# Performance work log

Measured on AMD Instinct MI355X. Metric: run time of the kernel, lower is better.

## Reference

```python
import jax, jax.numpy as jnp
import numpy as np

D_MODEL = 512
D_INNER = 1024   # expand * d_model
NH = 16          # heads (headdim 64)
HD = 64
NS = 16          # d_state
HID = 1024       # ff hidden = expand * d_model


def _ln(x, w, b, eps=1e-5):
    m = x.mean(-1, keepdims=True)
    v = ((x - m) ** 2).mean(-1, keepdims=True)
    return (x - m) * jax.lax.rsqrt(v + eps) * w + b


def _rms(x, w, eps=1e-5):
    return x * jax.lax.rsqrt((x * x).mean(-1, keepdims=True) + eps) * w


def _tree_scan(dt, xh, Bv, Cv, pidx, A):
    # dt:[B,T,W,H] xh:[B,T,W,H,P] Bv,Cv:[B,T,W,N] pidx:[B,T,W] A:[H]
    B_, T, W, H = dt.shape
    P = xh.shape[-1]
    N = Bv.shape[-1]
    h0 = jnp.zeros((B_, W, H, P, N), dt.dtype)
    xs = (jnp.moveaxis(dt, 1, 0), jnp.moveaxis(xh, 1, 0),
          jnp.moveaxis(Bv, 1, 0), jnp.moveaxis(Cv, 1, 0),
          jnp.moveaxis(pidx, 1, 0))

    def step(h, inp):
        dt_t, xh_t, b_t, c_t, p_t = inp
        # gather parent state from previous level along the width axis
        hp = jnp.take_along_axis(h, p_t[:, :, None, None, None], axis=1)  # [B,W,H,P,N]
        dA = jnp.exp(dt_t * A)                                            # [B,W,H]
        h_new = dA[..., None, None] * hp \
              + dt_t[..., None, None] * xh_t[..., None] * b_t[:, :, None, None, :]
        y_t = jnp.einsum('bwhpn,bwn->bwhp', h_new, c_t)
        return h_new, y_t

    _, ys = jax.lax.scan(step, h0, xs)
    return jnp.moveaxis(ys, 0, 1)  # [B,T,W,H,P]


def setup_inputs() -> dict:
    key = jax.random.key(0)
    ks = jax.random.split(key, 12)
    B, T, W = 8, 64, 16
    d_in_proj = 2 * D_INNER + 2 * NS + NH  # z | x | B | C | dt
    inp = {
        'x': jax.random.normal(ks[0], (B, T, W, D_MODEL), jnp.float32),
        'parent_pos': jax.random.randint(ks[1], (B, T, W), 0, W, dtype=jnp.int32),
        'ln1_w': jnp.ones((D_MODEL,), jnp.float32),
        'ln1_b': jnp.zeros((D_MODEL,), jnp.float32),
        'in_w': jax.random.normal(ks[2], (D_MODEL, d_in_proj), jnp.float32) * 0.02,
        'in_b': jnp.zeros((d_in_proj,), jnp.float32),
        'A_log': jnp.log(jax.random.uniform(ks[3], (NH,), jnp.float32, 1.0, 16.0)),
        'dt_bias': jnp.full((NH,), -4.0, jnp.float32),
        'Dp': jnp.ones((NH,), jnp.float32),
        'norm_w': jnp.ones((D_INNER,), jnp.float32),
        'out_w': jax.random.normal(ks[4], (D_INNER, D_MODEL), jnp.float32) * 0.02,
        'out_b': jnp.zeros((D_MODEL,), jnp.float32),
        'ln2_w': jnp.ones((D_MODEL,), jnp.float32),
        'ln2_b': jnp.zeros((D_MODEL,), jnp.float32),
        'ff1_w': jax.random.normal(ks[5], (D_MODEL, 2 * HID), jnp.float32) * 0.02,
        'ff1_b': jnp.zeros((2 * HID,), jnp.float32),
        'ff2_w': jax.random.normal(ks[6], (HID, D_MODEL), jnp.float32) * 0.02,
        'ff2_b': jnp.zeros((D_MODEL,), jnp.float32),
    }
    return inp


def reference(x, parent_pos, ln1_w, ln1_b, in_w, in_b, A_log, dt_bias, Dp,
              norm_w, out_w, out_b, ln2_w, ln2_b, ff1_w, ff1_b, ff2_w, ff2_b):
    # norm1 + TreeMamba2 + residual
    xn = _ln(x, ln1_w, ln1_b)
    proj = xn @ in_w + in_b
    z, xp, Bv, Cv, dtr = jnp.split(
        proj, [D_INNER, 2 * D_INNER, 2 * D_INNER + NS, 2 * D_INNER + 2 * NS], axis=-1)
    dt = jax.nn.softplus(dtr + dt_bias)            # [B,T,W,NH]
    A = -jnp.exp(A_log)                            # [NH]
    xh = xp.reshape(*xp.shape[:-1], NH, HD)        # [B,T,W,NH,HD]
    y = _tree_scan(dt, xh, Bv, Cv, parent_pos, A)  # [B,T,W,NH,HD]
    y = y + Dp[..., None] * xh                     # skip connection D*x
    y = y.reshape(*y.shape[:-2], D_INNER)
    y = _rms(y * jax.nn.silu(z), norm_w)           # gated RMSNorm
    y = y @ out_w + out_b
    x = y + x
    # norm2 + gated FF + residual
    yn = _ln(x, ln2_w, ln2_b)
    f = yn @ ff1_w + ff1_b
    f1, g = jnp.split(f, 2, axis=-1)
    f = (f1 * jax.nn.silu(g)) @ ff2_w + ff2_b
    return x + f
```

## Files before the change

### kernel.cpp

```cpp
#include <hip/hip_runtime.h>
#include <hip/hip_bf16.h>
#include <cmath>

#define D_MODEL 512
#define D_INNER 1024
#define NHEAD 16
#define HDIM 64
#define NSTATE 16
#define NB 8
#define NT 64
#define NW 16
#define MROWS 8192
#define PROJ_LD 2176
#define NPROJ 2096

typedef __attribute__((ext_vector_type(8))) short short8;
typedef __attribute__((ext_vector_type(4))) float f32x4;
typedef __hip_bfloat16 bf16;
typedef unsigned int u32;

__device__ __forceinline__ u32 fbits(float f) { return __float_as_uint(f); }
__device__ __forceinline__ float ubits(u32 u) { return __uint_as_float(u); }
__device__ __forceinline__ u32 pack_bf(float a, float b) {
  return (fbits(b) & 0xffff0000u) | (fbits(a) >> 16);
}

__device__ __forceinline__ float block_sum(float v, float* sbuf) {
#pragma unroll
  for (int o = 32; o > 0; o >>= 1) v += __shfl_down(v, o, 64);
  int lane = threadIdx.x & 63, wid = threadIdx.x >> 6;
  if (lane == 0) sbuf[wid] = v;
  __syncthreads();
  if (threadIdx.x == 0) {
    float t = 0.f;
    for (int i = 0; i < 4; i++) t += sbuf[i];
    sbuf[0] = t;
  }
  __syncthreads();
  return sbuf[0];
}

__global__ __launch_bounds__(256) void ln512_bf16_kernel(
    const float* __restrict__ x, const float* __restrict__ w,
    const float* __restrict__ b, bf16* __restrict__ out) {
  __shared__ float s1[8], s2[8];
  int row = blockIdx.x;
  const float* xr = x + (size_t)row * D_MODEL;
  bf16* outr = out + (size_t)row * D_MODEL;
  int c0 = threadIdx.x, c1 = threadIdx.x + 256;
  float v0 = xr[c0], v1 = xr[c1];
  float s  = block_sum(v0 + v1, s1);
  float ss = block_sum(v0 * v0 + v1 * v1, s2);
  float mean = s * (1.f / 512.f);
  float var  = ss * (1.f / 512.f) - mean * mean;
  float inv  = rsqrtf(var + 1e-5f);
  outr[c0] = __float2bfloat16((v0 - mean) * inv * w[c0] + b[c0]);
  outr[c1] = __float2bfloat16((v1 - mean) * inv * w[c1] + b[c1]);
}

__global__ __launch_bounds__(256) void wconv_t_kernel(
    const float* __restrict__ w, bf16* __restrict__ wt,
    int K, int N, int Npad) {
  __shared__ float tile[32][33];
  int n0 = blockIdx.x * 32, k0 = blockIdx.y * 32;
  int tx = threadIdx.x & 31, ty = threadIdx.x >> 5;
#pragma unroll
  for (int i = 0; i < 4; i++) {
    int k = k0 + ty + i * 8, n = n0 + tx;
    tile[ty + i * 8][tx] = (k < K && n < N) ? w[(size_t)k * N + n] : 0.f;
  }
  __syncthreads();
#pragma unroll
  for (int i = 0; i < 4; i++) {
    int n = n0 + ty + i * 8, k = k0 + tx;
    if (n < Npad && k < K) wt[(size_t)n * K + k] = __float2bfloat16(tile[tx][ty + i * 8]);
  }
}

template<int BM, int BN, int WN, int MR, int NR>
__global__ __launch_bounds__(256) void mfma_gemm_kernel(
    const bf16* __restrict__ A, const bf16* __restrict__ Bt,
    const float* __restrict__ bias, int nbias,
    const float* __restrict__ resid,
    float* __restrict__ C, int ldc, int K) {
  constexpr int ROWS = BM + BN;
  constexpr int ISS  = ROWS / 64;
  __shared__ __align__(16) bf16 sAB[2][ROWS][32];

  int wid = threadIdx.x >> 6, lane = threadIdx.x & 63;
  int row0 = blockIdx.y * BM, col0 = blockIdx.x * BN;
  int wr = (wid / WN) * (MR * 16);
  int wc = (wid % WN) * (NR * 16);
  int lr = lane >> 2;
  int lc = (lane & 3) * 8;

  f32x4 acc[MR][NR];
#pragma unroll
  for (int m = 0; m < MR; m++)
#pragma unroll
    for (int n = 0; n < NR; n++) acc[m][n] = (f32x4){0.f, 0.f, 0.f, 0.f};

  auto stage = [&](int buf, int k0) {
#pragma unroll
    for (int i = 0; i < ISS; i++) {
      int rb = (wid * ISS + i) * 16;
      int r = rb + lr;
      const bf16* src = (r < BM)
          ? A  + (size_t)(row0 + r) * K + k0 + lc
          : Bt + (size_t)(col0 + (r - BM)) * K + k0 + lc;
      __builtin_amdgcn_global_load_lds(
          (const __attribute__((address_space(1))) void*)src,
          (__attribute__((address_space(3))) void*)&sAB[buf][rb][0], 16, 0, 0);
    }
  };

  stage(0, 0);
  asm volatile("s_waitcnt vmcnt(0)" ::: "memory");
  __syncthreads();

  int cur = 0;
  for (int k0 = 0; k0 < K; k0 += 32, cur ^= 1) {
    if (k0 + 32 < K) stage(cur ^ 1, k0 + 32);
    short8 a[MR], b[NR];
    int kk = (lane >> 4) * 8;
#pragma unroll
    for (int m = 0; m < MR; m++)
      a[m] = *(const short8*)&sAB[cur][wr + m * 16 + (lane & 15)][kk];
#pragma unroll
    for (int n = 0; n < NR; n++)
      b[n] = *(const short8*)&sAB[cur][BM + wc + n * 16 + (lane & 15)][kk];
#pragma unroll
    for (int m = 0; m < MR; m++)
#pragma unroll
      for (int n = 0; n < NR; n++)
        acc[m][n] = __builtin_amdgcn_mfma_f32_16x16x32_bf16(a[m], b[n], acc[m][n], 0, 0, 0);
    asm volatile("s_waitcnt vmcnt(0)" ::: "memory");
    __syncthreads();
  }

  int crow = row0 + wr + (lane >> 4) * 4;
  int ccol = col0 + wc + (lane & 15);
#pragma unroll
  for (int m = 0; m < MR; m++) {
#pragma unroll
    for (int n = 0; n < NR; n++) {
      int colg = ccol + n * 16;
      float bv = bias ? ((colg < nbias) ? bias[colg] : 0.f) : 0.f;
#pragma unroll
      for (int j = 0; j < 4; j++) {
        int rowg = crow + m * 16 + j;
        float v = acc[m][n][j] + bv;
        if (resid) v += resid[(size_t)rowg * ldc + colg];
        C[(size_t)rowg * ldc + colg] = v;
      }
    }
  }
}

__global__ __launch_bounds__(256) void inproj_gemm_kernel(
    const bf16* __restrict__ A, const bf16* __restrict__ Bt,
    const float* __restrict__ bias,
    bf16* __restrict__ Cb, float* __restrict__ aux, int K) {
  constexpr int BM = 128, ROWS = 256, ISS = 4;
  __shared__ __align__(16) bf16 sAB[2][ROWS][32];

  int wid = threadIdx.x >> 6, lane = threadIdx.x & 63;
  int row0 = blockIdx.y * BM, col0 = blockIdx.x * 128;
  int wr = (wid >> 1) * 64;
  int wc = (wid & 1) * 64;
  int lr = lane >> 2;
  int lc = (lane & 3) * 8;

  f32x4 acc[4][4];
#pragma unroll
  for (int m = 0; m < 4; m++)
#pragma unroll
    for (int n = 0; n < 4; n++) acc[m][n] = (f32x4){0.f, 0.f, 0.f, 0.f};

  auto stage = [&](int buf, int k0) {
#pragma unroll
    for (int i = 0; i < ISS; i++) {
      int rb = (wid * ISS + i) * 16;
      int r = rb + lr;
      const bf16* src = (r < BM)
          ? A  + (size_t)(row0 + r) * K + k0 + lc
          : Bt + (size_t)(col0 + (r - BM)) * K + k0 + lc;
      __builtin_amdgcn_global_load_lds(
          (const __attribute__((address_space(1))) void*)src,
          (__attribute__((address_space(3))) void*)&sAB[buf][rb][0], 16, 0, 0);
    }
  };

  stage(0, 0);
  asm volatile("s_waitcnt vmcnt(0)" ::: "memory");
  __syncthreads();

  int cur = 0;
  for (int k0 = 0; k0 < K; k0 += 32, cur ^= 1) {
    if (k0 + 32 < K) stage(cur ^ 1, k0 + 32);
    short8 a[4], b[4];
    int kk = (lane >> 4) * 8;
#pragma unroll
    for (int m = 0; m < 4; m++)
      a[m] = *(const short8*)&sAB[cur][wr + m * 16 + (lane & 15)][kk];
#pragma unroll
    for (int n = 0; n < 4; n++)
      b[n] = *(const short8*)&sAB[cur][BM + wc + n * 16 + (lane & 15)][kk];
#pragma unroll
    for (int m = 0; m < 4; m++)
#pragma unroll
      for (int n = 0; n < 4; n++)
        acc[m][n] = __builtin_amdgcn_mfma_f32_16x16x32_bf16(a[m], b[n], acc[m][n], 0, 0, 0);
    asm volatile("s_waitcnt vmcnt(0)" ::: "memory");
    __syncthreads();
  }

  int crow = row0 + wr + (lane >> 4) * 4;
  int ccol = col0 + wc + (lane & 15);
#pragma unroll
  for (int m = 0; m < 4; m++) {
#pragma unroll
    for (int n = 0; n < 4; n++) {
      int colg = ccol + n * 16;
      float bv = (colg < NPROJ) ? bias[colg] : 0.f;
#pragma unroll
      for (int j = 0; j < 4; j++) {
        int rowg = crow + m * 16 + j;
        float v = acc[m][n][j] + bv;
        Cb[(size_t)rowg * PROJ_LD + colg] = __float2bfloat16(v);
        if (colg >= 2048 && colg < 2112)
          aux[(size_t)rowg * 64 + (colg - 2048)] = v;
      }
    }
  }
}

__global__ __launch_bounds__(256) void ff1_fused_kernel(
    const bf16* __restrict__ A, const bf16* __restrict__ Bt,
    const float* __restrict__ bias, bf16* __restrict__ out, int K) {
  constexpr int BM = 128, ROWS = 384, ISS = 6;
  __shared__ __align__(16) bf16 sAB[2][ROWS][32];

  int wid = threadIdx.x >> 6, lane = threadIdx.x & 63;
  int row0 = blockIdx.y * BM, col0 = blockIdx.x * 128;
  int wr = (wid >> 1) * 64;
  int wc = (wid & 1) * 64;
  int lr = lane >> 2;
  int lc = (lane & 3) * 8;

  f32x4 acc1[4][4], acc2[4][4];
#pragma unroll
  for (int m = 0; m < 4; m++)
#pragma unroll
    for (int n = 0; n < 4; n++) {
      acc1[m][n] = (f32x4){0.f, 0.f, 0.f, 0.f};
      acc2[m][n] = (f32x4){0.f, 0.f, 0.f, 0.f};
    }

  auto stage = [&](int buf, int k0) {
#pragma unroll
    for (int i = 0; i < ISS; i++) {
      int rb = (wid * ISS + i) * 16;
      int r = rb + lr;
      const bf16* src;
      if (r < BM)       src = A  + (size_t)(row0 + r) * K + k0 + lc;
      else if (r < 256) src = Bt + (size_t)(col0 + (r - 128)) * K + k0 + lc;
      else              src = Bt + (size_t)(1024 + col0 + (r - 256)) * K + k0 + lc;
      __builtin_amdgcn_global_load_lds(
          (const __attribute__((address_space(1))) void*)src,
          (__attribute__((address_space(3))) void*)&sAB[buf][rb][0], 16, 0, 0);
    }
  };

  stage(0, 0);
  asm volatile("s_waitcnt vmcnt(0)" ::: "memory");
  __syncthreads();

  int cur = 0;
  for (int k0 = 0; k0 < K; k0 += 32, cur ^= 1) {
    if (k0 + 32 < K) stage(cur ^ 1, k0 + 32);
    short8 a[4], b1[4], b2[4];
    int kk = (lane >> 4) * 8;
#pragma unroll
    for (int m = 0; m < 4; m++)
      a[m] = *(const short8*)&sAB[cur][wr + m * 16 + (lane & 15)][kk];
#pragma unroll
    for (int n = 0; n < 4; n++) {
      b1[n] = *(const short8*)&sAB[cur][128 + wc + n * 16 + (lane & 15)][kk];
      b2[n] = *(const short8*)&sAB[cur][256 + wc + n * 16 + (lane & 15)][kk];
    }
#pragma unroll
    for (int m = 0; m < 4; m++)
#pragma unroll
      for (int n = 0; n < 4; n++) {
        acc1[m][n] = __builtin_amdgcn_mfma_f32_16x16x32_bf16(a[m], b1[n], acc1[m][n], 0, 0, 0);
        acc2[m][n] = __builtin_amdgcn_mfma_f32_16x16x32_bf16(a[m], b2[n], acc2[m][n], 0, 0, 0);
      }
    asm volatile("s_waitcnt vmcnt(0)" ::: "memory");
    __syncthreads();
  }

  int crow = row0 + wr + (lane >> 4) * 4;
  int ccol = col0 + wc + (lane & 15);
#pragma unroll
  for (int m = 0; m < 4; m++) {
#pragma unroll
    for (int n = 0; n < 4; n++) {
      int colg = ccol + n * 16;
      float bv1 = bias[colg];
      float bv2 = bias[1024 + colg];
#pragma unroll
      for (int j = 0; j < 4; j++) {
        int rowg = crow + m * 16 + j;
        float f1 = acc1[m][n][j] + bv1;
        float g  = acc2[m][n][j] + bv2;
        float sg = g / (1.f + expf(-g));
        out[(size_t)rowg * 1024 + colg] = __float2bfloat16(f1 * sg);
      }
    }
  }
}

__global__ __launch_bounds__(256) void tree_scan_kernel(
    const bf16* __restrict__ xb, const float* __restrict__ aux,
    const int* __restrict__ parent,
    const float* __restrict__ A_log, const float* __restrict__ dt_bias,
    const float* __restrict__ Dp, bf16* __restrict__ y) {
  const int tid = threadIdx.x;
  const int ps = blockIdx.x & 3;
  const int h  = (blockIdx.x >> 2) & 15;
  const int b  = blockIdx.x >> 6;
  const int wid = tid >> 6;
  const int lane = tid & 63;
  const int w = lane >> 2;
  const int q = lane & 3;
  const int pl = wid * 4 + q;

  __shared__ __align__(16) u32   BCs[8][16][20];
  __shared__ __align__(16) float dAs[16][8];
  __shared__ __align__(16) float dtss[16][8];
  __shared__ __align__(16) int   pars[16][8];

  const float Ah  = -expf(A_log[h]);
  const float dtb = dt_bias[h];
  const float Dh  = Dp[h];
  const int xcol = 1024 + (h << 6) + (ps << 4) + pl;
  const int ycol = (h << 6) + (ps << 4) + pl;

  float hst[16];
#pragma unroll
  for (int n = 0; n < 16; n++) hst[n] = 0.f;

  const int sp_t = (tid >> 1) >> 4, sp_w = (tid >> 1) & 15, sp_h = tid & 1;

  for (int c = 0; c < 8; c++) {
    const int t0 = c * 8;
    __syncthreads();
    float xv[8];
#pragma unroll
    for (int tt = 0; tt < 8; tt++) {
      size_t row = ((size_t)(b * NT + t0 + tt)) * NW + w;
      xv[tt] = __bfloat162float(xb[row * PROJ_LD + xcol]);
    }
    if (tid < 128) {
      int t = tid >> 4, wv = tid & 15;
      size_t row = ((size_t)(b * NT + t0 + t)) * NW + wv;
      float dtr = aux[row * 64 + 32 + h] + dtb;
      float dtv = (dtr > 20.f) ? dtr : log1pf(expf(dtr));
      dtss[wv][t] = dtv;
      dAs[wv][t]  = expf(dtv * Ah);
      pars[wv][t] = parent[row];
    }
    {
      size_t row = ((size_t)(b * NT + t0 + sp_t)) * NW + sp_w;
      const float* src = aux + row * 64 + sp_h * 16;
      float4 v0 = *(const float4*)&src[0];
      float4 v1 = *(const float4*)&src[4];
      float4 v2 = *(const float4*)&src[8];
      float4 v3 = *(const float4*)&src[12];
      uint4 p0 = {pack_bf(v0.x, v0.y), pack_bf(v0.z, v0.w),
                  pack_bf(v1.x, v1.y), pack_bf(v1.z, v1.w)};
      uint4 p1 = {pack_bf(v2.x, v2.y), pack_bf(v2.z, v2.w),
                  pack_bf(v3.x, v3.y), pack_bf(v3.z, v3.w)};
      *(uint4*)&BCs[sp_t][sp_w][sp_h * 8]     = p0;
      *(uint4*)&BCs[sp_t][sp_w][sp_h * 8 + 4] = p1;
    }
    __syncthreads();
    float dAr[8], dtr8[8];
    int parr[8];
    *(float4*)&dAr[0]  = *(const float4*)&dAs[w][0];
    *(float4*)&dAr[4]  = *(const float4*)&dAs[w][4];
    *(float4*)&dtr8[0] = *(const float4*)&dtss[w][0];
    *(float4*)&dtr8[4] = *(const float4*)&dtss[w][4];
    *(int4*)&parr[0]   = *(const int4*)&pars[w][0];
    *(int4*)&parr[4]   = *(const int4*)&pars[w][4];

#pragma unroll
    for (int tt = 0; tt < 8; tt++) {
      float dA  = dAr[tt];
      float dtx = dtr8[tt] * xv[tt];
      int   par = parr[tt];
      int gidx = (((par << 2) | q) << 2);
      u32 pk[8];
#pragma unroll
      for (int i = 0; i < 8; i++)
        pk[i] = (u32)__builtin_amdgcn_ds_bpermute(
            gidx, (int)pack_bf(hst[2 * i], hst[2 * i + 1]));
      uint4 bA = *(const uint4*)&BCs[tt][w][0];
      uint4 bB = *(const uint4*)&BCs[tt][w][4];
      uint4 cA = *(const uint4*)&BCs[tt][w][8];
      uint4 cB = *(const uint4*)&BCs[tt][w][12];
      const u32* bw = (const u32*)&bA;
      u32 bwv[8] = {bA.x, bA.y, bA.z, bA.w, bB.x, bB.y, bB.z, bB.w};
      u32 cwv[8] = {cA.x, cA.y, cA.z, cA.w, cB.x, cB.y, cB.z, cB.w};
      (void)bw;
      float yv = 0.f;
#pragma unroll
      for (int i = 0; i < 8; i++) {
        u32 g = pk[i], bu = bwv[i], cu = cwv[i];
        float hp0 = ubits(g << 16),  hp1 = ubits(g & 0xffff0000u);
        float bl  = ubits(bu << 16), bh  = ubits(bu & 0xffff0000u);
        float cl  = ubits(cu << 16), ch  = ubits(cu & 0xffff0000u);
        float h0 = fmaf(dA, hp0, dtx * bl);
        float h1 = fmaf(dA, hp1, dtx * bh);
        hst[2 * i] = h0;
        hst[2 * i + 1] = h1;
        yv = fmaf(h0, cl, fmaf(h1, ch, yv));
      }
      size_t row = ((size_t)(b * NT + t0 + tt)) * NW + w;
      y[row * D_INNER + ycol] = __float2bfloat16(fmaf(Dh, xv[tt], yv));
    }
  }
}

__global__ __launch_bounds__(256) void gate_rms_kernel(
    const bf16* __restrict__ yin, const bf16* __restrict__ projb,
    const float* __restrict__ norm_w, bf16* __restrict__ out) {
  __shared__ float sbuf[8];
  int row = blockIdx.x;
  const bf16* yr = yin + (size_t)row * D_INNER;
  const bf16* zr = projb + (size_t)row * PROJ_LD;
  int c = threadIdx.x * 4;
  bf16 y4[4], z4[4];
  *(uint2*)y4 = *(const uint2*)&yr[c];
  *(uint2*)z4 = *(const uint2*)&zr[c];
  float gv[4];
  float ss = 0.f;
#pragma unroll
  for (int j = 0; j < 4; j++) {
    float z = __bfloat162float(z4[j]);
    float t = __bfloat162float(y4[j]) * (z / (1.f + expf(-z)));
    gv[j] = t;
    ss += t * t;
  }
  ss = block_sum(ss, sbuf);
  float scale = rsqrtf(ss * (1.f / 1024.f) + 1e-5f);
  bf16 o4[4];
#pragma unroll
  for (int j = 0; j < 4; j++) o4[j] = __float2bfloat16(gv[j] * scale * norm_w[c + j]);
  *(uint2*)&out[(size_t)row * D_INNER + c] = *(uint2*)o4;
}

extern "C" void kernel_launch(void* const* d_in, const int* in_sizes, int n_in,
                              void* d_out, int out_size, void* d_ws, size_t ws_size,
                              hipStream_t stream) {
  const float* x       = (const float*)d_in[0];
  const int*   parent  = (const int*)d_in[1];
  const float* ln1_w   = (const float*)d_in[2];
  const float* ln1_b   = (const float*)d_in[3];
  const float* in_w    = (const float*)d_in[4];
  const float* in_b    = (const float*)d_in[5];
  const float* A_log   = (const float*)d_in[6];
  const float* dt_bias = (const float*)d_in[7];
  const float* Dp      = (const float*)d_in[8];
  const float* norm_w  = (const float*)d_in[9];
  const float* out_w   = (const float*)d_in[10];
  const float* out_b   = (const float*)d_in[11];
  const float* ln2_w   = (const float*)d_in[12];
  const float* ln2_b   = (const float*)d_in[13];
  const float* ff1_w   = (const float*)d_in[14];
  const float* ff1_b   = (const float*)d_in[15];
  const float* ff2_w   = (const float*)d_in[16];
  const float* ff2_b   = (const float*)d_in[17];
  float* outp = (float*)d_out;

  char* wp = (char*)d_ws;
  bf16* xnb    = (bf16*)wp;  wp += (size_t)MROWS * D_MODEL * 2;
  bf16* in_wt  = (bf16*)wp;  wp += (size_t)PROJ_LD * D_MODEL * 2;
  bf16* out_wt = (bf16*)wp;  wp += (size_t)D_MODEL * D_INNER * 2;
  bf16* ff1_wt = (bf16*)wp;  wp += (size_t)2048 * D_MODEL * 2;
  bf16* ff2_wt = (bf16*)wp;  wp += (size_t)D_MODEL * D_INNER * 2;
  bf16* projb  = (bf16*)wp;  wp += (size_t)MROWS * PROJ_LD * 2;
  float* aux   = (float*)wp; wp += (size_t)MROWS * 64 * 4;
  bf16* yb     = (bf16*)wp;  wp += (size_t)MROWS * D_INNER * 2;
  bf16* ygb    = (bf16*)wp;  wp += (size_t)MROWS * D_INNER * 2;
  float* xmid  = outp;

  dim3 blk(256);
  wconv_t_kernel<<<dim3(PROJ_LD / 32, D_MODEL / 32), blk, 0, stream>>>(
      in_w, in_wt, D_MODEL, NPROJ, PROJ_LD);
  wconv_t_kernel<<<dim3(D_MODEL / 32, D_INNER / 32), blk, 0, stream>>>(
      out_w, out_wt, D_INNER, D_MODEL, D_MODEL);
  wconv_t_kernel<<<dim3(2048 / 32, D_MODEL / 32), blk, 0, stream>>>(
      ff1_w, ff1_wt, D_MODEL, 2048, 2048);
  wconv_t_kernel<<<dim3(D_MODEL / 32, D_INNER / 32), blk, 0, stream>>>(
      ff2_w, ff2_wt, D_INNER, D_MODEL, D_MODEL);

  ln512_bf16_kernel<<<MROWS, blk, 0, stream>>>(x, ln1_w, ln1_b, xnb);
  inproj_gemm_kernel<<<dim3(PROJ_LD / 128, MROWS / 128), blk, 0, stream>>>(
      xnb, in_wt, in_b, projb, aux, D_MODEL);
  tree_scan_kernel<<<NB * NHEAD * 4, blk, 0, stream>>>(projb, aux, parent,
                                                       A_log, dt_bias, Dp, yb);
  gate_rms_kernel<<<MROWS, blk, 0, stream>>>(yb, projb, norm_w, ygb);
  mfma_gemm_kernel<64, 128, 4, 4, 2><<<dim3(D_MODEL / 128, MROWS / 64), blk, 0, stream>>>(
      ygb, out_wt, out_b, D_MODEL, x, xmid, D_MODEL, D_INNER);
  ln512_bf16_kernel<<<MROWS, blk, 0, stream>>>(xmid, ln2_w, ln2_b, xnb);
  ff1_fused_kernel<<<dim3(8, MROWS / 128), blk, 0, stream>>>(
      xnb, ff1_wt, ff1_b, ygb, D_MODEL);
  mfma_gemm_kernel<64, 128, 4, 4, 2><<<dim3(D_MODEL / 128, MROWS / 64), blk, 0, stream>>>(
      ygb, ff2_wt, ff2_b, D_MODEL, xmid, outp, D_MODEL, D_INNER);
}
```

Measured before the change: 218.2 us.

## Split tree scan across state-dimension halves and sum partial outputs in gate-RMS

The tree scan grid doubles so that each block handles half of the 16 SSM state entries. This halves per-thread state registers, bpermutes and B/C loads. Each half writes a partial y to its own buffer, the D skip term is added only by the first half, and gate_rms_kernel sums the two partials before gating. This raises parallelism for the latency-bound scan, at the cost of an extra 16MB bf16 buffer write and read and a second rounding of y to bf16.

```diff
diff --git a/kernel.cpp b/kernel.cpp
--- a/kernel.cpp
+++ b/kernel.cpp
@@ -325,33 +325,36 @@
     const bf16* __restrict__ xb, const float* __restrict__ aux,
     const int* __restrict__ parent,
     const float* __restrict__ A_log, const float* __restrict__ dt_bias,
-    const float* __restrict__ Dp, bf16* __restrict__ y) {
+    const float* __restrict__ Dp, bf16* __restrict__ y0,
+    bf16* __restrict__ y1) {
   const int tid = threadIdx.x;
-  const int ps = blockIdx.x & 3;
-  const int h  = (blockIdx.x >> 2) & 15;
-  const int b  = blockIdx.x >> 6;
+  const int nh = blockIdx.x & 1;
+  const int ps = (blockIdx.x >> 1) & 3;
+  const int h  = (blockIdx.x >> 3) & 15;
+  const int b  = blockIdx.x >> 7;
   const int wid = tid >> 6;
   const int lane = tid & 63;
   const int w = lane >> 2;
   const int q = lane & 3;
   const int pl = wid * 4 + q;
 
-  __shared__ __align__(16) u32   BCs[8][16][20];
+  __shared__ __align__(16) u32   BCs[8][16][12];
   __shared__ __align__(16) float dAs[16][8];
   __shared__ __align__(16) float dtss[16][8];
   __shared__ __align__(16) int   pars[16][8];
 
   const float Ah  = -expf(A_log[h]);
   const float dtb = dt_bias[h];
-  const float Dh  = Dp[h];
+  const float Dh  = nh ? 0.f : Dp[h];
   const int xcol = 1024 + (h << 6) + (ps << 4) + pl;
   const int ycol = (h << 6) + (ps << 4) + pl;
-
-  float hst[16];
-#pragma unroll
-  for (int n = 0; n < 16; n++) hst[n] = 0.f;
-
-  const int sp_t = (tid >> 1) >> 4, sp_w = (tid >> 1) & 15, sp_h = tid & 1;
+  bf16* __restrict__ yout = nh ? y1 : y0;
+
+  float hst[8];
+#pragma unroll
+  for (int n = 0; n < 8; n++) hst[n] = 0.f;
+
+  const int sg_t = tid >> 5, sg_w = (tid >> 1) & 15, sg_h = tid & 1;
 
   for (int c = 0; c < 8; c++) {
     const int t0 = c * 8;
@@ -372,18 +375,13 @@
       pars[wv][t] = parent[row];
     }
     {
-      size_t row = ((size_t)(b * NT + t0 + sp_t)) * NW + sp_w;
-      const float* src = aux + row * 64 + sp_h * 16;
+      size_t row = ((size_t)(b * NT + t0 + sg_t)) * NW + sg_w;
+      const float* src = aux + row * 64 + sg_h * 16 + nh * 8;
       float4 v0 = *(const float4*)&src[0];
       float4 v1 = *(const float4*)&src[4];
-      float4 v2 = *(const float4*)&src[8];
-      float4 v3 = *(const float4*)&src[12];
-      uint4 p0 = {pack_bf(v0.x, v0.y), pack_bf(v0.z, v0.w),
-                  pack_bf(v1.x, v1.y), pack_bf(v1.z, v1.w)};
-      uint4 p1 = {pack_bf(v2.x, v2.y), pack_bf(v2.z, v2.w),
-                  pack_bf(v3.x, v3.y), pack_bf(v3.z, v3.w)};
-      *(uint4*)&BCs[sp_t][sp_w][sp_h * 8]     = p0;
-      *(uint4*)&BCs[sp_t][sp_w][sp_h * 8 + 4] = p1;
+      uint4 p = {pack_bf(v0.x, v0.y), pack_bf(v0.z, v0.w),
+                 pack_bf(v1.x, v1.y), pack_bf(v1.z, v1.w)};
+      *(uint4*)&BCs[sg_t][sg_w][sg_h * 4] = p;
     }
     __syncthreads();
     float dAr[8], dtr8[8];
@@ -401,22 +399,18 @@
       float dtx = dtr8[tt] * xv[tt];
       int   par = parr[tt];
       int gidx = (((par << 2) | q) << 2);
-      u32 pk[8];
-#pragma unroll
-      for (int i = 0; i < 8; i++)
+      u32 pk[4];
+#pragma unroll
+      for (int i = 0; i < 4; i++)
         pk[i] = (u32)__builtin_amdgcn_ds_bpermute(
             gidx, (int)pack_bf(hst[2 * i], hst[2 * i + 1]));
-      uint4 bA = *(const uint4*)&BCs[tt][w][0];
-      uint4 bB = *(const uint4*)&BCs[tt][w][4];
-      uint4 cA = *(const uint4*)&BCs[tt][w][8];
-      uint4 cB = *(const uint4*)&BCs[tt][w][12];
-      const u32* bw = (const u32*)&bA;
-      u32 bwv[8] = {bA.x, bA.y, bA.z, bA.w, bB.x, bB.y, bB.z, bB.w};
-      u32 cwv[8] = {cA.x, cA.y, cA.z, cA.w, cB.x, cB.y, cB.z, cB.w};
-      (void)bw;
+      uint4 bu4 = *(const uint4*)&BCs[tt][w][0];
+      uint4 cu4 = *(const uint4*)&BCs[tt][w][4];
+      u32 bwv[4] = {bu4.x, bu4.y, bu4.z, bu4.w};
+      u32 cwv[4] = {cu4.x, cu4.y, cu4.z, cu4.w};
       float yv = 0.f;
 #pragma unroll
-      for (int i = 0; i < 8; i++) {
+      for (int i = 0; i < 4; i++) {
         u32 g = pk[i], bu = bwv[i], cu = cwv[i];
         float hp0 = ubits(g << 16),  hp1 = ubits(g & 0xffff0000u);
         float bl  = ubits(bu << 16), bh  = ubits(bu & 0xffff0000u);
@@ -428,28 +422,32 @@
         yv = fmaf(h0, cl, fmaf(h1, ch, yv));
       }
       size_t row = ((size_t)(b * NT + t0 + tt)) * NW + w;
-      y[row * D_INNER + ycol] = __float2bfloat16(fmaf(Dh, xv[tt], yv));
+      yout[row * D_INNER + ycol] = __float2bfloat16(fmaf(Dh, xv[tt], yv));
     }
   }
 }
 
 __global__ __launch_bounds__(256) void gate_rms_kernel(
-    const bf16* __restrict__ yin, const bf16* __restrict__ projb,
+    const bf16* __restrict__ y0, const bf16* __restrict__ y1,
+    const bf16* __restrict__ projb,
     const float* __restrict__ norm_w, bf16* __restrict__ out) {
   __shared__ float sbuf[8];
   int row = blockIdx.x;
-  const bf16* yr = yin + (size_t)row * D_INNER;
+  const bf16* yr0 = y0 + (size_t)row * D_INNER;
+  const bf16* yr1 = y1 + (size_t)row * D_INNER;
   const bf16* zr = projb + (size_t)row * PROJ_LD;
   int c = threadIdx.x * 4;
-  bf16 y4[4], z4[4];
-  *(uint2*)y4 = *(const uint2*)&yr[c];
+  bf16 a4[4], b4[4], z4[4];
+  *(uint2*)a4 = *(const uint2*)&yr0[c];
+  *(uint2*)b4 = *(const uint2*)&yr1[c];
   *(uint2*)z4 = *(const uint2*)&zr[c];
   float gv[4];
   float ss = 0.f;
 #pragma unroll
   for (int j = 0; j < 4; j++) {
     float z = __bfloat162float(z4[j]);
-    float t = __bfloat162float(y4[j]) * (z / (1.f + expf(-z)));
+    float yv = __bfloat162float(a4[j]) + __bfloat162float(b4[j]);
+    float t = yv * (z / (1.f + expf(-z)));
     gv[j] = t;
     ss += t * t;
   }
@@ -492,7 +490,8 @@
   bf16* ff2_wt = (bf16*)wp;  wp += (size_t)D_MODEL * D_INNER * 2;
   bf16* projb  = (bf16*)wp;  wp += (size_t)MROWS * PROJ_LD * 2;
   float* aux   = (float*)wp; wp += (size_t)MROWS * 64 * 4;
-  bf16* yb     = (bf16*)wp;  wp += (size_t)MROWS * D_INNER * 2;
+  bf16* yb0    = (bf16*)wp;  wp += (size_t)MROWS * D_INNER * 2;
+  bf16* yb1    = (bf16*)wp;  wp += (size_t)MROWS * D_INNER * 2;
   bf16* ygb    = (bf16*)wp;  wp += (size_t)MROWS * D_INNER * 2;
   float* xmid  = outp;
 
@@ -509,9 +508,9 @@
   ln512_bf16_kernel<<<MROWS, blk, 0, stream>>>(x, ln1_w, ln1_b, xnb);
   inproj_gemm_kernel<<<dim3(PROJ_LD / 128, MROWS / 128), blk, 0, stream>>>(
       xnb, in_wt, in_b, projb, aux, D_MODEL);
-  tree_scan_kernel<<<NB * NHEAD * 4, blk, 0, stream>>>(projb, aux, parent,
-                                                       A_log, dt_bias, Dp, yb);
-  gate_rms_kernel<<<MROWS, blk, 0, stream>>>(yb, projb, norm_w, ygb);
+  tree_scan_kernel<<<NB * NHEAD * 4 * 2, blk, 0, stream>>>(
+      projb, aux, parent, A_log, dt_bias, Dp, yb0, yb1);
+  gate_rms_kernel<<<MROWS, blk, 0, stream>>>(yb0, yb1, projb, norm_w, ygb);
   mfma_gemm_kernel<64, 128, 4, 4, 2><<<dim3(D_MODEL / 128, MROWS / 64), blk, 0, stream>>>(
       ygb, out_wt, out_b, D_MODEL, x, xmid, D_MODEL, D_INNER);
   ln512_bf16_kernel<<<MROWS, blk, 0, stream>>>(xmid, ln2_w, ln2_b, xnb);
```

Result: slower. 223.6 us (+2.5%).

## Fuse gated RMSNorm, out-projection, residual and LayerNorm2 into one kernel

Applied to the files above, without the earlier changes.

Replaces gate_rms, the out-proj GEMM and the second LayerNorm with one kernel that uses full-width 512-column tiles. Each tile computes y*silu(z) on the fly, accumulates the RMS sum of squares during A staging, and applies the RMS scale per row in the epilogue. norm_w is folded into the transposed out_w during weight conversion. The epilogue adds bias and residual, writes xmid, and computes LayerNorm2 in-block to emit the bf16 input for ff1. The four weight conversion launches are merged into one, and the ygb buffer is dropped by reusing yb. This cuts launches and intermediate global traffic, at the cost of a grid of only 256 blocks with a large B tile that may limit occupancy.

```diff
diff --git a/kernel.cpp b/kernel.cpp
--- a/kernel.cpp
+++ b/kernel.cpp
@@ -58,11 +58,21 @@
   outr[c1] = __float2bfloat16((v1 - mean) * inv * w[c1] + b[c1]);
 }
 
-__global__ __launch_bounds__(256) void wconv_t_kernel(
-    const float* __restrict__ w, bf16* __restrict__ wt,
-    int K, int N, int Npad) {
+__global__ __launch_bounds__(256) void wconv_all_kernel(
+    const float* __restrict__ in_w, bf16* __restrict__ in_wt,
+    const float* __restrict__ out_w, bf16* __restrict__ out_wt,
+    const float* __restrict__ norm_w,
+    const float* __restrict__ ff1_w, bf16* __restrict__ ff1_wt,
+    const float* __restrict__ ff2_w, bf16* __restrict__ ff2_wt) {
   __shared__ float tile[32][33];
-  int n0 = blockIdx.x * 32, k0 = blockIdx.y * 32;
+  int id = blockIdx.x;
+  const float* w; bf16* wt; const float* sc = nullptr;
+  int K, N, Npad, bx, by;
+  if (id < 1088)      { w = in_w;  wt = in_wt;  K = 512;  N = NPROJ; Npad = PROJ_LD; bx = id % 68;  by = id / 68; }
+  else if (id < 1600) { int j = id - 1088; w = out_w; wt = out_wt; sc = norm_w; K = 1024; N = 512;  Npad = 512;  bx = j % 16; by = j / 16; }
+  else if (id < 2624) { int j = id - 1600; w = ff1_w; wt = ff1_wt; K = 512;  N = 2048; Npad = 2048; bx = j % 64; by = j / 64; }
+  else                { int j = id - 2624; w = ff2_w; wt = ff2_wt; K = 1024; N = 512;  Npad = 512;  bx = j % 16; by = j / 16; }
+  int n0 = bx * 32, k0 = by * 32;
   int tx = threadIdx.x & 31, ty = threadIdx.x >> 5;
 #pragma unroll
   for (int i = 0; i < 4; i++) {
@@ -70,10 +80,12 @@
     tile[ty + i * 8][tx] = (k < K && n < N) ? w[(size_t)k * N + n] : 0.f;
   }
   __syncthreads();
+  float s = sc ? sc[k0 + tx] : 1.f;
 #pragma unroll
   for (int i = 0; i < 4; i++) {
     int n = n0 + ty + i * 8, k = k0 + tx;
-    if (n < Npad && k < K) wt[(size_t)n * K + k] = __float2bfloat16(tile[tx][ty + i * 8]);
+    if (n < Npad && k < K)
+      wt[(size_t)n * K + k] = __float2bfloat16(tile[tx][ty + i * 8] * s);
   }
 }
 
@@ -316,6 +328,147 @@
         float g  = acc2[m][n][j] + bv2;
         float sg = g / (1.f + expf(-g));
         out[(size_t)rowg * 1024 + colg] = __float2bfloat16(f1 * sg);
+      }
+    }
+  }
+}
+
+__global__ __launch_bounds__(256) void outproj_fused_kernel(
+    const bf16* __restrict__ yb, const bf16* __restrict__ projb,
+    const bf16* __restrict__ Wt, const float* __restrict__ out_b,
+    const float* __restrict__ x, const float* __restrict__ ln2w,
+    const float* __restrict__ ln2b,
+    float* __restrict__ xmid, bf16* __restrict__ xnb) {
+  constexpr int BM = 32, BN = 512, K = 1024;
+  __shared__ __align__(16) bf16 Ab[2][BM][32];
+  __shared__ __align__(16) bf16 Bb[2][BN][32];
+  __shared__ float srow[BM];
+  __shared__ float2 red[BM][4];
+
+  const int tid = threadIdx.x, wid = tid >> 6, lane = tid & 63;
+  const int row0 = blockIdx.x * BM;
+  const int wc = wid * 128;
+  const int lr = lane >> 2, lc4 = (lane & 3) * 8;
+  const int ar = tid >> 3, akc = (tid & 7) * 4;
+
+  f32x4 acc[2][8];
+#pragma unroll
+  for (int m = 0; m < 2; m++)
+#pragma unroll
+    for (int n = 0; n < 8; n++) acc[m][n] = (f32x4){0.f, 0.f, 0.f, 0.f};
+  float ssp = 0.f;
+
+  auto stageB = [&](int buf, int k0) {
+#pragma unroll
+    for (int i = 0; i < 8; i++) {
+      int rb = (wid * 8 + i) * 16;
+      const bf16* src = Wt + (size_t)(rb + lr) * K + k0 + lc4;
+      __builtin_amdgcn_global_load_lds(
+          (const __attribute__((address_space(1))) void*)src,
+          (__attribute__((address_space(3))) void*)&Bb[buf][rb][0], 16, 0, 0);
+    }
+  };
+  uint2 yv, zv;
+  auto loadA = [&](int k0) {
+    yv = *(const uint2*)&yb[(size_t)(row0 + ar) * D_INNER + k0 + akc];
+    zv = *(const uint2*)&projb[(size_t)(row0 + ar) * PROJ_LD + k0 + akc];
+  };
+  auto writeA = [&](int buf) {
+    bf16 ya[4], za[4];
+    *(uint2*)ya = yv;
+    *(uint2*)za = zv;
+    float t[4];
+#pragma unroll
+    for (int j = 0; j < 4; j++) {
+      float z = __bfloat162float(za[j]);
+      t[j] = __bfloat162float(ya[j]) * (z / (1.f + expf(-z)));
+      ssp += t[j] * t[j];
+    }
+    bf16 tb[4];
+#pragma unroll
+    for (int j = 0; j < 4; j++) tb[j] = __float2bfloat16(t[j]);
+    *(uint2*)&Ab[buf][ar][akc] = *(uint2*)tb;
+  };
+
+  stageB(0, 0);
+  loadA(0);
+  asm volatile("s_waitcnt vmcnt(0)" ::: "memory");
+  writeA(0);
+  __syncthreads();
+
+  int cur = 0;
+  for (int k0 = 0; k0 < K; k0 += 32, cur ^= 1) {
+    bool more = (k0 + 32 < K);
+    if (more) { stageB(cur ^ 1, k0 + 32); loadA(k0 + 32); }
+    short8 a[2], b[8];
+    int kk = (lane >> 4) * 8;
+#pragma unroll
+    for (int m = 0; m < 2; m++)
+      a[m] = *(const short8*)&Ab[cur][m * 16 + (lane & 15)][kk];
+#pragma unroll
+    for (int n = 0; n < 8; n++)
+      b[n] = *(const short8*)&Bb[cur][wc + n * 16 + (lane & 15)][kk];
+#pragma unroll
+    for (int m = 0; m < 2; m++)
+#pragma unroll
+      for (int n = 0; n < 8; n++)
+        acc[m][n] = __builtin_amdgcn_mfma_f32_16x16x32_bf16(a[m], b[n], acc[m][n], 0, 0, 0);
+    if (more) {
+      asm volatile("s_waitcnt vmcnt(0)" ::: "memory");
+      writeA(cur ^ 1);
+    }
+    __syncthreads();
+  }
+
+#pragma unroll
+  for (int o = 1; o < 8; o <<= 1) ssp += __shfl_xor(ssp, o, 8);
+  if ((lane & 7) == 0) srow[ar] = rsqrtf(ssp * (1.f / 1024.f) + 1e-5f);
+  __syncthreads();
+
+  const int cl = lane & 15, rj = (lane >> 4) * 4;
+#pragma unroll
+  for (int m = 0; m < 2; m++) {
+#pragma unroll
+    for (int j = 0; j < 4; j++) {
+      int row = m * 16 + rj + j;
+      int grow = row0 + row;
+      float sr = srow[row];
+      float s = 0.f, q = 0.f;
+#pragma unroll
+      for (int n = 0; n < 8; n++) {
+        int col = wc + n * 16 + cl;
+        float v = acc[m][n][j] * sr + out_b[col] + x[(size_t)grow * 512 + col];
+        acc[m][n][j] = v;
+        xmid[(size_t)grow * 512 + col] = v;
+        s += v;
+        q += v * v;
+      }
+#pragma unroll
+      for (int o = 1; o < 16; o <<= 1) {
+        s += __shfl_xor(s, o, 16);
+        q += __shfl_xor(q, o, 16);
+      }
+      if (cl == 0) red[row][wid] = make_float2(s, q);
+    }
+  }
+  __syncthreads();
+#pragma unroll
+  for (int m = 0; m < 2; m++) {
+#pragma unroll
+    for (int j = 0; j < 4; j++) {
+      int row = m * 16 + rj + j;
+      int grow = row0 + row;
+      float2 r0 = red[row][0], r1 = red[row][1], r2 = red[row][2], r3 = red[row][3];
+      float sum = r0.x + r1.x + r2.x + r3.x;
+      float sq  = r0.y + r1.y + r2.y + r3.y;
+      float mean = sum * (1.f / 512.f);
+      float var  = sq * (1.f / 512.f) - mean * mean;
+      float inv  = rsqrtf(var + 1e-5f);
+#pragma unroll
+      for (int n = 0; n < 8; n++) {
+        int col = wc + n * 16 + cl;
+        float xnv = (acc[m][n][j] - mean) * inv * ln2w[col] + ln2b[col];
+        xnb[(size_t)grow * 512 + col] = __float2bfloat16(xnv);
       }
     }
   }
@@ -410,10 +563,8 @@
       uint4 bB = *(const uint4*)&BCs[tt][w][4];
       uint4 cA = *(const uint4*)&BCs[tt][w][8];
       uint4 cB = *(const uint4*)&BCs[tt][w][12];
-      const u32* bw = (const u32*)&bA;
       u32 bwv[8] = {bA.x, bA.y, bA.z, bA.w, bB.x, bB.y, bB.z, bB.w};
       u32 cwv[8] = {cA.x, cA.y, cA.z, cA.w, cB.x, cB.y, cB.z, cB.w};
-      (void)bw;
       float yv = 0.f;
 #pragma unroll
       for (int i = 0; i < 8; i++) {
@@ -431,34 +582,6 @@
       y[row * D_INNER + ycol] = __float2bfloat16(fmaf(Dh, xv[tt], yv));
     }
   }
-}
-
-__global__ __launch_bounds__(256) void gate_rms_kernel(
-    const bf16* __restrict__ yin, const bf16* __restrict__ projb,
-    const float* __restrict__ norm_w, bf16* __restrict__ out) {
-  __shared__ float sbuf[8];
-  int row = blockIdx.x;
-  const bf16* yr = yin + (size_t)row * D_INNER;
-  const bf16* zr = projb + (size_t)row * PROJ_LD;
-  int c = threadIdx.x * 4;
-  bf16 y4[4], z4[4];
-  *(uint2*)y4 = *(const uint2*)&yr[c];
-  *(uint2*)z4 = *(const uint2*)&zr[c];
-  float gv[4];
-  float ss = 0.f;
-#pragma unroll
-  for (int j = 0; j < 4; j++) {
-    float z = __bfloat162float(z4[j]);
-    float t = __bfloat162float(y4[j]) * (z / (1.f + expf(-z)));
-    gv[j] = t;
-    ss += t * t;
-  }
-  ss = block_sum(ss, sbuf);
-  float scale = rsqrtf(ss * (1.f / 1024.f) + 1e-5f);
-  bf16 o4[4];
-#pragma unroll
-  for (int j = 0; j < 4; j++) o4[j] = __float2bfloat16(gv[j] * scale * norm_w[c + j]);
-  *(uint2*)&out[(size_t)row * D_INNER + c] = *(uint2*)o4;
 }
 
 extern "C" void kernel_launch(void* const* d_in, const int* in_sizes, int n_in,
@@ -493,30 +616,20 @@
   bf16* projb  = (bf16*)wp;  wp += (size_t)MROWS * PROJ_LD * 2;
   float* aux   = (float*)wp; wp += (size_t)MROWS * 64 * 4;
   bf16* yb     = (bf16*)wp;  wp += (size_t)MROWS * D_INNER * 2;
-  bf16* ygb    = (bf16*)wp;  wp += (size_t)MROWS * D_INNER * 2;
   float* xmid  = outp;
 
   dim3 blk(256);
-  wconv_t_kernel<<<dim3(PROJ_LD / 32, D_MODEL / 32), blk, 0, stream>>>(
-      in_w, in_wt, D_MODEL, NPROJ, PROJ_LD);
-  wconv_t_kernel<<<dim3(D_MODEL / 32, D_INNER / 32), blk, 0, stream>>>(
-      out_w, out_wt, D_INNER, D_MODEL, D_MODEL);
-  wconv_t_kernel<<<dim3(2048 / 32, D_MODEL / 32), blk, 0, stream>>>(
-      ff1_w, ff1_wt, D_MODEL, 2048, 2048);
-  wconv_t_kernel<<<dim3(D_MODEL / 32, D_INNER / 32), blk, 0, stream>>>(
-      ff2_w, ff2_wt, D_INNER, D_MODEL, D_MODEL);
-
+  wconv_all_kernel<<<3136, blk, 0, stream>>>(
+      in_w, in_wt, out_w, out_wt, norm_w, ff1_w, ff1_wt, ff2_w, ff2_wt);
   ln512_bf16_kernel<<<MROWS, blk, 0, stream>>>(x, ln1_w, ln1_b, xnb);
   inproj_gemm_kernel<<<dim3(PROJ_LD / 128, MROWS / 128), blk, 0, stream>>>(
       xnb, in_wt, in_b, projb, aux, D_MODEL);
   tree_scan_kernel<<<NB * NHEAD * 4, blk, 0, stream>>>(projb, aux, parent,
                                                        A_log, dt_bias, Dp, yb);
-  gate_rms_kernel<<<MROWS, blk, 0, stream>>>(yb, projb, norm_w, ygb);
+  outproj_fused_kernel<<<MROWS / 32, blk, 0, stream>>>(
+      yb, projb, out_wt, out_b, x, ln2_w, ln2_b, xmid, xnb);
+  ff1_fused_kernel<<<dim3(8, MROWS / 128), blk, 0, stream>>>(
+      xnb, ff1_wt, ff1_b, yb, D_MODEL);
   mfma_gemm_kernel<64, 128, 4, 4, 2><<<dim3(D_MODEL / 128, MROWS / 64), blk, 0, stream>>>(
-      ygb, out_wt, out_b, D_MODEL, x, xmid, D_MODEL, D_INNER);
-  ln512_bf16_kernel<<<MROWS, blk, 0, stream>>>(xmid, ln2_w, ln2_b, xnb);
-  ff1_fused_kernel<<<dim3(8, MROWS / 128), blk, 0, stream>>>(
-      xnb, ff1_wt, ff1_b, ygb, D_MODEL);
-  mfma_gemm_kernel<64, 128, 4, 4, 2><<<dim3(D_MODEL / 128, MROWS / 64), blk, 0, stream>>>(
-      ygb, ff2_wt, ff2_b, D_MODEL, xmid, outp, D_MODEL, D_INNER);
-}
+      yb, ff2_wt, ff2_b, D_MODEL, xmid, outp, D_MODEL, D_INNER);
+}
```

Measured after the change: 217.7 us. Within noise of the previous version (-0.2%).

## Triple-buffer GEMM K-loop staging and merge weight conversion launches

Applied to the files above, without the earlier changes.

All three MFMA GEMM kernels move from double to triple buffering in shared memory. Loads run two K-steps ahead, and each iteration does one partial vmcnt wait plus one barrier instead of a full drain and a trailing barrier. This is meant to hide global-to-LDS latency behind the MFMA work. The four weight transpose-convert launches are merged into one kernel that picks its weight by block index, cutting launch overhead. The cost is more LDS per block, which may lower occupancy, especially in the FF1 kernel.

```diff
diff --git a/kernel.cpp b/kernel.cpp
--- a/kernel.cpp
+++ b/kernel.cpp
@@ -23,6 +23,16 @@
 __device__ __forceinline__ float ubits(u32 u) { return __uint_as_float(u); }
 __device__ __forceinline__ u32 pack_bf(float a, float b) {
   return (fbits(b) & 0xffff0000u) | (fbits(a) >> 16);
+}
+
+template<int N> __device__ __forceinline__ void vmwait() {
+  if constexpr (N == 0)      asm volatile("s_waitcnt vmcnt(0)" ::: "memory");
+  else if constexpr (N == 2) asm volatile("s_waitcnt vmcnt(2)" ::: "memory");
+  else if constexpr (N == 3) asm volatile("s_waitcnt vmcnt(3)" ::: "memory");
+  else if constexpr (N == 4) asm volatile("s_waitcnt vmcnt(4)" ::: "memory");
+  else if constexpr (N == 6) asm volatile("s_waitcnt vmcnt(6)" ::: "memory");
+  else if constexpr (N == 8) asm volatile("s_waitcnt vmcnt(8)" ::: "memory");
+  else static_assert(N == 0, "unsupported vmcnt");
 }
 
 __device__ __forceinline__ float block_sum(float v, float* sbuf) {
@@ -58,11 +68,20 @@
   outr[c1] = __float2bfloat16((v1 - mean) * inv * w[c1] + b[c1]);
 }
 
-__global__ __launch_bounds__(256) void wconv_t_kernel(
-    const float* __restrict__ w, bf16* __restrict__ wt,
-    int K, int N, int Npad) {
+__global__ __launch_bounds__(256) void wconv_all_kernel(
+    const float* __restrict__ in_w, bf16* __restrict__ in_wt,
+    const float* __restrict__ out_w, bf16* __restrict__ out_wt,
+    const float* __restrict__ ff1_w, bf16* __restrict__ ff1_wt,
+    const float* __restrict__ ff2_w, bf16* __restrict__ ff2_wt) {
   __shared__ float tile[32][33];
-  int n0 = blockIdx.x * 32, k0 = blockIdx.y * 32;
+  int id = blockIdx.x;
+  const float* w; bf16* wt;
+  int K, N, Npad, bx, by;
+  if (id < 1088)      { w = in_w;  wt = in_wt;  K = 512;  N = NPROJ; Npad = PROJ_LD; bx = id % 68;  by = id / 68; }
+  else if (id < 1600) { int j = id - 1088; w = out_w; wt = out_wt; K = 1024; N = 512;  Npad = 512;  bx = j % 16; by = j / 16; }
+  else if (id < 2624) { int j = id - 1600; w = ff1_w; wt = ff1_wt; K = 512;  N = 2048; Npad = 2048; bx = j % 64; by = j / 64; }
+  else                { int j = id - 2624; w = ff2_w; wt = ff2_wt; K = 1024; N = 512;  Npad = 512;  bx = j % 16; by = j / 16; }
+  int n0 = bx * 32, k0 = by * 32;
   int tx = threadIdx.x & 31, ty = threadIdx.x >> 5;
 #pragma unroll
   for (int i = 0; i < 4; i++) {
@@ -73,7 +92,8 @@
 #pragma unroll
   for (int i = 0; i < 4; i++) {
     int n = n0 + ty + i * 8, k = k0 + tx;
-    if (n < Npad && k < K) wt[(size_t)n * K + k] = __float2bfloat16(tile[tx][ty + i * 8]);
+    if (n < Npad && k < K)
+      wt[(size_t)n * K + k] = __float2bfloat16(tile[tx][ty + i * 8]);
   }
 }
 
@@ -85,7 +105,7 @@
     float* __restrict__ C, int ldc, int K) {
   constexpr int ROWS = BM + BN;
   constexpr int ISS  = ROWS / 64;
-  __shared__ __align__(16) bf16 sAB[2][ROWS][32];
+  __shared__ __align__(16) bf16 sAB[3][ROWS][32];
 
   int wid = threadIdx.x >> 6, lane = threadIdx.x & 63;
   int row0 = blockIdx.y * BM, col0 = blockIdx.x * BN;
@@ -115,12 +135,13 @@
   };
 
   stage(0, 0);
-  asm volatile("s_waitcnt vmcnt(0)" ::: "memory");
-  __syncthreads();
-
+  stage(1, 32);
   int cur = 0;
-  for (int k0 = 0; k0 < K; k0 += 32, cur ^= 1) {
-    if (k0 + 32 < K) stage(cur ^ 1, k0 + 32);
+  for (int k0 = 0; k0 < K; k0 += 32) {
+    if (k0 + 32 < K) vmwait<ISS>(); else vmwait<0>();
+    __builtin_amdgcn_s_barrier();
+    asm volatile("" ::: "memory");
+    if (k0 + 64 < K) stage(cur == 0 ? 2 : cur - 1, k0 + 64);
     short8 a[MR], b[NR];
     int kk = (lane >> 4) * 8;
 #pragma unroll
@@ -134,8 +155,8 @@
 #pragma unroll
       for (int n = 0; n < NR; n++)
         acc[m][n] = __builtin_amdgcn_mfma_f32_16x16x32_bf16(a[m], b[n], acc[m][n], 0, 0, 0);
-    asm volatile("s_waitcnt vmcnt(0)" ::: "memory");
-    __syncthreads();
+    asm volatile("" ::: "memory");
+    cur = (cur == 2) ? 0 : cur + 1;
   }
 
   int crow = row0 + wr + (lane >> 4) * 4;
@@ -162,7 +183,7 @@
     const float* __restrict__ bias,
     bf16* __restrict__ Cb, float* __restrict__ aux, int K) {
   constexpr int BM = 128, ROWS = 256, ISS = 4;
-  __shared__ __align__(16) bf16 sAB[2][ROWS][32];
+  __shared__ __align__(16) bf16 sAB[3][ROWS][32];
 
   int wid = threadIdx.x >> 6, lane = threadIdx.x & 63;
   int row0 = blockIdx.y * BM, col0 = blockIdx.x * 128;
@@ -192,12 +213,13 @@
   };
 
   stage(0, 0);
-  asm volatile("s_waitcnt vmcnt(0)" ::: "memory");
-  __syncthreads();
-
+  stage(1, 32);
   int cur = 0;
-  for (int k0 = 0; k0 < K; k0 += 32, cur ^= 1) {
-    if (k0 + 32 < K) stage(cur ^ 1, k0 + 32);
+  for (int k0 = 0; k0 < K; k0 += 32) {
+    if (k0 + 32 < K) vmwait<ISS>(); else vmwait<0>();
+    __builtin_amdgcn_s_barrier();
+    asm volatile("" ::: "memory");
+    if (k0 + 64 < K) stage(cur == 0 ? 2 : cur - 1, k0 + 64);
     short8 a[4], b[4];
     int kk = (lane >> 4) * 8;
 #pragma unroll
@@ -211,8 +233,8 @@
 #pragma unroll
       for (int n = 0; n < 4; n++)
         acc[m][n] = __builtin_amdgcn_mfma_f32_16x16x32_bf16(a[m], b[n], acc[m][n], 0, 0, 0);
-    asm volatile("s_waitcnt vmcnt(0)" ::: "memory");
-    __syncthreads();
+    asm volatile("" ::: "memory");
+    cur = (cur == 2) ? 0 : cur + 1;
   }
 
   int crow = row0 + wr + (lane >> 4) * 4;
@@ -239,7 +261,7 @@
     const bf16* __restrict__ A, const bf16* __restrict__ Bt,
     const float* __restrict__ bias, bf16* __restrict__ out, int K) {
   constexpr int BM = 128, ROWS = 384, ISS = 6;
-  __shared__ __align__(16) bf16 sAB[2][ROWS][32];
+  __shared__ __align__(16) bf16 sAB[3][ROWS][32];
 
   int wid = threadIdx.x >> 6, lane = threadIdx.x & 63;
   int row0 = blockIdx.y * BM, col0 = blockIdx.x * 128;
@@ -273,12 +295,13 @@
   };
 
   stage(0, 0);
-  asm volatile("s_waitcnt vmcnt(0)" ::: "memory");
-  __syncthreads();
-
+  stage(1, 32);
   int cur = 0;
-  for (int k0 = 0; k0 < K; k0 += 32, cur ^= 1) {
-    if (k0 + 32 < K) stage(cur ^ 1, k0 + 32);
+  for (int k0 = 0; k0 < K; k0 += 32) {
+    if (k0 + 32 < K) vmwait<ISS>(); else vmwait<0>();
+    __builtin_amdgcn_s_barrier();
+    asm volatile("" ::: "memory");
+    if (k0 + 64 < K) stage(cur == 0 ? 2 : cur - 1, k0 + 64);
     short8 a[4], b1[4], b2[4];
     int kk = (lane >> 4) * 8;
 #pragma unroll
@@ -296,8 +319,8 @@
         acc1[m][n] = __builtin_amdgcn_mfma_f32_16x16x32_bf16(a[m], b1[n], acc1[m][n], 0, 0, 0);
         acc2[m][n] = __builtin_amdgcn_mfma_f32_16x16x32_bf16(a[m], b2[n], acc2[m][n], 0, 0, 0);
       }
-    asm volatile("s_waitcnt vmcnt(0)" ::: "memory");
-    __syncthreads();
+    asm volatile("" ::: "memory");
+    cur = (cur == 2) ? 0 : cur + 1;
   }
 
   int crow = row0 + wr + (lane >> 4) * 4;
@@ -410,15 +433,15 @@
       uint4 bB = *(const uint4*)&BCs[tt][w][4];
       uint4 cA = *(const uint4*)&BCs[tt][w][8];
       uint4 cB = *(const uint4*)&BCs[tt][w][12];
-      const u32* bw = (const u32*)&bA;
       u32 bwv[8] = {bA.x, bA.y, bA.z, bA.w, bB.x, bB.y, bB.z, bB.w};
       u32 cwv[8] = {cA.x, cA.y, cA.z, cA.w, cB.x, cB.y, cB.z, cB.w};
-      (void)bw;
       float yv = 0.f;
 #pragma unroll
       for (int i = 0; i < 8; i++) {
         u32 g = pk[i], bu = bwv[i], cu = cwv[i];
-        float hp0 = ubits(g << 16),  hp1 = ubits(g & 0xffff0000u);
+        float hp0 = ubits(g << 16),  float_hp1_dummy;
+        (void)float_hp1_dummy;
+        float hp1 = ubits(g & 0xffff0000u);
         float bl  = ubits(bu << 16), bh  = ubits(bu & 0xffff0000u);
         float cl  = ubits(cu << 16), ch  = ubits(cu & 0xffff0000u);
         float h0 = fmaf(dA, hp0, dtx * bl);
@@ -497,15 +520,8 @@
   float* xmid  = outp;
 
   dim3 blk(256);
-  wconv_t_kernel<<<dim3(PROJ_LD / 32, D_MODEL / 32), blk, 0, stream>>>(
-      in_w, in_wt, D_MODEL, NPROJ, PROJ_LD);
-  wconv_t_kernel<<<dim3(D_MODEL / 32, D_INNER / 32), blk, 0, stream>>>(
-      out_w, out_wt, D_INNER, D_MODEL, D_MODEL);
-  wconv_t_kernel<<<dim3(2048 / 32, D_MODEL / 32), blk, 0, stream>>>(
-      ff1_w, ff1_wt, D_MODEL, 2048, 2048);
-  wconv_t_kernel<<<dim3(D_MODEL / 32, D_INNER / 32), blk, 0, stream>>>(
-      ff2_w, ff2_wt, D_INNER, D_MODEL, D_MODEL);
-
+  wconv_all_kernel<<<3136, blk, 0, stream>>>(
+      in_w, in_wt, out_w, out_wt, ff1_w, ff1_wt, ff2_w, ff2_wt);
   ln512_bf16_kernel<<<MROWS, blk, 0, stream>>>(x, ln1_w, ln1_b, xnb);
   inproj_gemm_kernel<<<dim3(PROJ_LD / 128, MROWS / 128), blk, 0, stream>>>(
       xnb, in_wt, in_b, projb, aux, D_MODEL);
@@ -516,7 +532,7 @@
       ygb, out_wt, out_b, D_MODEL, x, xmid, D_MODEL, D_INNER);
   ln512_bf16_kernel<<<MROWS, blk, 0, stream>>>(xmid, ln2_w, ln2_b, xnb);
   ff1_fused_kernel<<<dim3(8, MROWS / 128), blk, 0, stream>>>(
-      xnb, ff1_wt, ff1_b, ygb, D_MODEL);
+      xnb, ff1_wt, ff1_b, yb, D_MODEL);
   mfma_gemm_kernel<64, 128, 4, 4, 2><<<dim3(D_MODEL / 128, MROWS / 64), blk, 0, stream>>>(
-      ygb, ff2_wt, ff2_b, D_MODEL, xmid, outp, D_MODEL, D_INNER);
-}
+      yb, ff2_wt, ff2_b, D_MODEL, xmid, outp, D_MODEL, D_INNER);
+}
```

Result: faster. 206.6 us (-5.3%).
